# Optimization experiments

Measured on AMD Instinct MI355X. Metric: run time of the kernel, lower is better.

The kernel has to match this reference:

```python
import jax, jax.numpy as jnp
import numpy as np

N = 50000        # nodes
E = 1600000      # edges (before self-loops)
HID = 128
HEADS = 4
HD = HID // HEADS
FIN = 32 + 7     # node feats + scenario feats
EPS = 1e-5


def _ln(x, g, b):
    m = x.mean(-1, keepdims=True)
    v = ((x - m) ** 2).mean(-1, keepdims=True)
    return (x - m) / jnp.sqrt(v + EPS) * g + b


def _gat(x, src, dst, W, a_s, a_d, bias):
    # PyG GATConv (concat=True, negative_slope=0.2), eval mode (no dropout)
    xp = (x @ W).reshape(-1, HEADS, HD)                    # [N,H,C]
    es = (xp * a_s).sum(-1)                                # [N,H]
    ed = (xp * a_d).sum(-1)                                # [N,H]
    e = jax.nn.leaky_relu(es[src] + ed[dst], 0.2)          # [Etot,H]
    emax = jax.ops.segment_max(e, dst, num_segments=N)     # per-target softmax (self-loops guarantee nonempty segments)
    a = jnp.exp(e - emax[dst])
    denom = jax.ops.segment_sum(a, dst, num_segments=N)
    a = a / denom[dst]
    out = jax.ops.segment_sum(xp[src] * a[:, :, None], dst, num_segments=N)
    return out.reshape(-1, HID) + bias


def setup_inputs() -> dict:
    key = jax.random.key(0)
    ks = iter(jax.random.split(key, 64))

    def rn(shape, scale=0.05):
        return jax.random.normal(next(ks), shape, dtype=jnp.float32) * scale

    inp = {}
    inp["x"] = jax.random.normal(next(ks), (N, FIN), dtype=jnp.float32)
    inp["edge_index"] = jax.random.randint(next(ks), (2, E), 0, N)
    inp["enc_w1"] = rn((FIN, HID)); inp["enc_b1"] = jnp.zeros((HID,), jnp.float32)
    inp["enc_w2"] = rn((HID, HID)); inp["enc_b2"] = jnp.zeros((HID,), jnp.float32)
    for l in (1, 2, 3):
        inp[f"W{l}"] = rn((HID, HID))
        inp[f"as{l}"] = rn((HEADS, HD))
        inp[f"ad{l}"] = rn((HEADS, HD))
        inp[f"bc{l}"] = jnp.zeros((HID,), jnp.float32)
        inp[f"g{l}"] = jnp.ones((HID,), jnp.float32)
        inp[f"be{l}"] = jnp.zeros((HID,), jnp.float32)
    inp["imp_w1"] = rn((HID, HID // 2)); inp["imp_b1"] = jnp.zeros((HID // 2,), jnp.float32)
    inp["imp_w2"] = rn((HID // 2, 3));   inp["imp_b2"] = jnp.zeros((3,), jnp.float32)
    inp["tim_w1"] = rn((HID, HID // 2)); inp["tim_b1"] = jnp.zeros((HID // 2,), jnp.float32)
    inp["tim_w2"] = rn((HID // 2, 2));   inp["tim_b2"] = jnp.zeros((2,), jnp.float32)
    return inp


def reference(x, edge_index, enc_w1, enc_b1, enc_w2, enc_b2,
              W1, as1, ad1, bc1, g1, be1,
              W2, as2, ad2, bc2, g2, be2,
              W3, as3, ad3, bc3, g3, be3,
              imp_w1, imp_b1, imp_w2, imp_b2,
              tim_w1, tim_b1, tim_w2, tim_b2):
    loops = jnp.arange(N, dtype=edge_index.dtype)          # add_self_loops=True
    src = jnp.concatenate([edge_index[0], loops])
    dst = jnp.concatenate([edge_index[1], loops])
    h = jax.nn.relu(x @ enc_w1 + enc_b1) @ enc_w2 + enc_b2
    for (W, a_s, a_d, bc, g, be) in ((W1, as1, ad1, bc1, g1, be1),
                                     (W2, as2, ad2, bc2, g2, be2),
                                     (W3, as3, ad3, bc3, g3, be3)):
        h = jax.nn.relu(_ln(_gat(h, src, dst, W, a_s, a_d, bc) + h, g, be))
    impact = jax.nn.relu(h @ imp_w1 + imp_b1) @ imp_w2 + imp_b2
    timing = jax.nn.softplus(jax.nn.relu(h @ tim_w1 + tim_b1) @ tim_w2 + tim_b2)
    return (impact, timing)
```

## Files before the change

### kernel.cpp

```cpp
#include <hip/hip_runtime.h>
#include <hip/hip_bf16.h>
#include <math.h>

#define NN 50000
#define EDGES 1600000
#define ETOT (EDGES + NN)
#define FINDIM 39
#define NPART 256
#define PSZ 196
#define PCAP 7100
#define P1TILE 4096

typedef __attribute__((ext_vector_type(8))) short short8;
typedef __attribute__((ext_vector_type(4))) float floatx4;

__device__ __forceinline__ unsigned pack_bf16(float a, float b) {
    __hip_bfloat162 t;
    t.x = __float2bfloat16(a);
    t.y = __float2bfloat16(b);
    return *(unsigned*)&t;
}
__device__ __forceinline__ float2 unpack_bf16(unsigned w) {
    float2 r;
    r.x = __uint_as_float(w << 16);
    r.y = __uint_as_float(w & 0xffff0000u);
    return r;
}

__device__ __forceinline__ int src_at(const int* ei, int i, bool i32) {
    return i32 ? ei[i] : ei[2 * i];
}
__device__ __forceinline__ int dst_at(const int* ei, int i, bool i32) {
    return i32 ? ei[EDGES + i] : ei[2 * (EDGES + i)];
}

__global__ __launch_bounds__(1024) void pass1_kernel(const int* __restrict__ ei,
                                                     int* __restrict__ gcursor,
                                                     unsigned* __restrict__ pbuf) {
    __shared__ unsigned raw[P1TILE];
    __shared__ unsigned srt[P1TILE];
    __shared__ int pcnt[NPART], poff[NPART], pcur[NPART], gb[NPART];
    __shared__ int i32flag;
    int t = threadIdx.x;
    if (t == 0) i32flag = 0;
    __syncthreads();
    int chunk = (ETOT + gridDim.x - 1) / gridDim.x;
    int c0 = blockIdx.x * chunk;
    int c1 = c0 + chunk; if (c1 > ETOT) c1 = ETOT;
    int sb = c0 < EDGES - 64 ? c0 : 0;
    if (t < 64 && ei[2 * (sb + t) + 1] != 0) i32flag = 1;
    __syncthreads();
    bool i32 = (i32flag != 0);
    for (int t0 = c0; t0 < c1; t0 += P1TILE) {
        int tn = c1 - t0; if (tn > P1TILE) tn = P1TILE;
        if (t < NPART) { pcnt[t] = 0; pcur[t] = 0; }
        __syncthreads();
        for (int i = t; i < tn; i += 1024) {
            int e = t0 + i;
            int s, d;
            if (e < EDGES) { s = src_at(ei, e, i32); d = dst_at(ei, e, i32); }
            else { s = d = e - EDGES; }
            raw[i] = ((unsigned)s << 16) | (unsigned)d;
            atomicAdd(&pcnt[d / PSZ], 1);
        }
        __syncthreads();
        if (t < NPART) poff[t] = pcnt[t];
        __syncthreads();
        for (int off = 1; off < NPART; off <<= 1) {
            int v = (t < NPART && t >= off) ? poff[t - off] : 0;
            __syncthreads();
            if (t < NPART) poff[t] += v;
            __syncthreads();
        }
        if (t < NPART) {
            poff[t] -= pcnt[t];
            gb[t] = atomicAdd(&gcursor[t], pcnt[t]);
        }
        __syncthreads();
        for (int i = t; i < tn; i += 1024) {
            unsigned r = raw[i];
            int part = (int)(r & 0xFFFFu) / PSZ;
            int pos = poff[part] + atomicAdd(&pcur[part], 1);
            srt[pos] = r;
        }
        __syncthreads();
        for (int i = t; i < tn; i += 1024) {
            unsigned r = srt[i];
            int part = (int)(r & 0xFFFFu) / PSZ;
            int gpos = gb[part] + (i - poff[part]);
            if (gpos < PCAP) pbuf[(size_t)part * PCAP + gpos] = r;
        }
        __syncthreads();
    }
}

__global__ __launch_bounds__(1024) void pass2_kernel(const unsigned* __restrict__ pbuf,
                                                     const int* __restrict__ gcursor,
                                                     int* __restrict__ rowptr,
                                                     int* __restrict__ colidx) {
    __shared__ unsigned recs[PCAP];
    __shared__ int lhist[PSZ], lexcl[PSZ], lcur[PSZ];
    __shared__ int psm[NPART];
    int p = blockIdx.x;
    int t = threadIdx.x;
    if (t < NPART) psm[t] = gcursor[t];
    __syncthreads();
    for (int off = 1; off < NPART; off <<= 1) {
        int x = (t < NPART && t >= off) ? psm[t - off] : 0;
        __syncthreads();
        if (t < NPART) psm[t] += x;
        __syncthreads();
    }
    int n = gcursor[p]; if (n > PCAP) n = PCAP;
    int base = psm[p] - gcursor[p];
    if (p == NPART - 1 && t == 0) rowptr[NN] = psm[NPART - 1];
    int d0 = p * PSZ;
    int nd = NN - d0; if (nd > PSZ) nd = PSZ;
    if (nd < 0) nd = 0;
    for (int i = t; i < nd; i += 1024) { lhist[i] = 0; lcur[i] = 0; }
    __syncthreads();
    for (int i = t; i < n; i += 1024) {
        unsigned r = pbuf[(size_t)p * PCAP + i];
        recs[i] = r;
        atomicAdd(&lhist[(int)(r & 0xFFFFu) - d0], 1);
    }
    __syncthreads();
    for (int i = t; i < nd; i += 1024) lexcl[i] = lhist[i];
    __syncthreads();
    for (int off = 1; off < PSZ; off <<= 1) {
        int a0 = 0;
        if (t < nd && t >= off) a0 = lexcl[t - off];
        __syncthreads();
        if (t < nd) lexcl[t] += a0;
        __syncthreads();
    }
    for (int i = t; i < nd; i += 1024) {
        lexcl[i] -= lhist[i];
        rowptr[d0 + i] = base + lexcl[i];
    }
    __syncthreads();
    for (int i = t; i < n; i += 1024) {
        unsigned r = recs[i];
        int li = (int)(r & 0xFFFFu) - d0;
        int pos = base + lexcl[li] + atomicAdd(&lcur[li], 1);
        colidx[pos] = (int)(r >> 16);
    }
}

template <int NC, bool RELU, int K>
__global__ __launch_bounds__(256) void gemm_small_kernel(const float* __restrict__ A,
                                                         const float* __restrict__ B,
                                                         const float* __restrict__ bias,
                                                         float* __restrict__ C, int M) {
    constexpr int TM = 32;
    constexpr int GROUPS = 256 / NC;
    constexpr int RPG = TM / GROUPS;
    constexpr int KC = 64;
    __shared__ float As[TM * 128];
    __shared__ float Bs[KC * NC];
    int t = threadIdx.x;
    int i0 = blockIdx.x * TM;

    int rows = M - i0; if (rows > TM) rows = TM;
    for (int idx = t; idx < rows * K; idx += 256) {
        int r = idx / K, k = idx - r * K;
        As[r * K + k] = A[(size_t)(i0 + r) * K + k];
    }

    int col = t % NC, grp = t / NC;
    int rg0 = grp * RPG;
    float acc[RPG];
#pragma unroll
    for (int r = 0; r < RPG; ++r) acc[r] = 0.f;

    for (int k0 = 0; k0 < K; k0 += KC) {
        int kc = K - k0; if (kc > KC) kc = KC;
        __syncthreads();
        for (int idx = t; idx < kc * NC; idx += 256) Bs[idx] = B[(size_t)k0 * NC + idx];
        __syncthreads();
        for (int k = 0; k < kc; ++k) {
            float bv = Bs[k * NC + col];
#pragma unroll
            for (int r = 0; r < RPG; ++r) acc[r] += As[(rg0 + r) * K + k0 + k] * bv;
        }
    }

    float bb = bias ? bias[col] : 0.f;
#pragma unroll
    for (int r = 0; r < RPG; ++r) {
        int i = i0 + rg0 + r;
        if (i < M) {
            float v = acc[r] + bb;
            if (RELU) v = v > 0.f ? v : 0.f;
            C[(size_t)i * NC + col] = v;
        }
    }
}

__global__ __launch_bounds__(256) void wconv5_kernel(const float* __restrict__ W0,
                                                     const float* __restrict__ W1,
                                                     const float* __restrict__ W2,
                                                     const float* __restrict__ ew2,
                                                     const float* __restrict__ iw1,
                                                     const float* __restrict__ tw1,
                                                     unsigned short* __restrict__ wtb,
                                                     int* __restrict__ gcursor) {
    if (blockIdx.x == 0 && threadIdx.x < NPART) gcursor[threadIdx.x] = 0;
    int idx = blockIdx.x * 256 + threadIdx.x;
    int m = idx >> 14;
    int r = idx & 16383;
    int c = r >> 7, k = r & 127;
    float v;
    if (m == 0) v = W0[(size_t)k * 128 + c];
    else if (m == 1) v = W1[(size_t)k * 128 + c];
    else if (m == 2) v = W2[(size_t)k * 128 + c];
    else if (m == 3) v = ew2[(size_t)k * 128 + c];
    else v = (c < 64) ? iw1[(size_t)k * 64 + c] : tw1[(size_t)k * 64 + (c - 64)];
    unsigned p = pack_bf16(v, 0.f);
    wtb[idx] = (unsigned short)(p & 0xffffu);
}

__device__ __forceinline__ void mfma_core(const float* __restrict__ A, int arow, int valid,
                                          const unsigned short* __restrict__ wtb,
                                          int c, int grp, floatx4 acc[8]) {
#pragma unroll
    for (int n = 0; n < 8; ++n) acc[n] = (floatx4){0.f, 0.f, 0.f, 0.f};
    short8 af[4];
#pragma unroll
    for (int kc = 0; kc < 4; ++kc) {
        float4 f0 = make_float4(0.f, 0.f, 0.f, 0.f), f1 = f0;
        if (valid) {
            const float* hp = &A[(size_t)arow * 128 + (kc << 5) + (grp << 3)];
            f0 = *(const float4*)hp;
            f1 = *(const float4*)(hp + 4);
        }
        unsigned pk[4];
        pk[0] = pack_bf16(f0.x, f0.y);
        pk[1] = pack_bf16(f0.z, f0.w);
        pk[2] = pack_bf16(f1.x, f1.y);
        pk[3] = pack_bf16(f1.z, f1.w);
        af[kc] = *(short8*)pk;
    }
#pragma unroll
    for (int kc = 0; kc < 4; ++kc) {
#pragma unroll
        for (int n = 0; n < 8; ++n) {
            short8 bf = *(const short8*)&wtb[(size_t)(((n << 4) + c) * 128 + (kc << 5) + (grp << 3))];
            acc[n] = __builtin_amdgcn_mfma_f32_16x16x32_bf16(af[kc], bf, acc[n], 0, 0, 0);
        }
    }
}

__global__ __launch_bounds__(256) void gemm_mfma_kernel(const float* __restrict__ H,
                                                        const unsigned short* __restrict__ wtb,
                                                        unsigned* __restrict__ XP,
                                                        const float* __restrict__ a_s,
                                                        const float* __restrict__ a_d,
                                                        float* __restrict__ es,
                                                        float* __restrict__ ed, int M) {
    int t = threadIdx.x;
    int w = t >> 6, l = t & 63;
    int c = l & 15, grp = l >> 4;
    int i0 = blockIdx.x * 64 + w * 16;
    int arow = i0 + c;

    floatx4 acc[8];
    mfma_core(H, arow, arow < M, wtb, c, grp, acc);

    float asv[8], adv[8];
#pragma unroll
    for (int n = 0; n < 8; ++n) { asv[n] = a_s[(n << 4) + c]; adv[n] = a_d[(n << 4) + c]; }

    float sp[4][4], dp[4][4];
#pragma unroll
    for (int r = 0; r < 4; ++r)
#pragma unroll
        for (int hd = 0; hd < 4; ++hd) { sp[r][hd] = 0.f; dp[r][hd] = 0.f; }

#pragma unroll
    for (int n = 0; n < 8; ++n) {
#pragma unroll
        for (int r = 0; r < 4; ++r) {
            float vv = acc[n][r];
            float pv = __shfl_xor(vv, 1);
            int row = i0 + (grp << 2) + r;
            if (!(c & 1) && row < M)
                XP[(size_t)row * 64 + (n << 3) + (c >> 1)] = pack_bf16(vv, pv);
            sp[r][n >> 1] = fmaf(vv, asv[n], sp[r][n >> 1]);
            dp[r][n >> 1] = fmaf(vv, adv[n], dp[r][n >> 1]);
        }
    }
#pragma unroll
    for (int r = 0; r < 4; ++r)
#pragma unroll
        for (int hd = 0; hd < 4; ++hd) {
            float s = sp[r][hd], d = dp[r][hd];
#pragma unroll
            for (int off = 1; off <= 8; off <<= 1) {
                s += __shfl_xor(s, off);
                d += __shfl_xor(d, off);
            }
            sp[r][hd] = s; dp[r][hd] = d;
        }
    if (c < 4) {
#pragma unroll
        for (int r = 0; r < 4; ++r) {
            int row = i0 + (grp << 2) + r;
            if (row < M) {
                float s = (c == 0) ? sp[r][0] : (c == 1) ? sp[r][1] : (c == 2) ? sp[r][2] : sp[r][3];
                float d = (c == 0) ? dp[r][0] : (c == 1) ? dp[r][1] : (c == 2) ? dp[r][2] : dp[r][3];
                es[(size_t)row * 4 + c] = s;
                ed[(size_t)row * 4 + c] = d;
            }
        }
    }
}

__global__ __launch_bounds__(256) void gemm_mfma_bias_kernel(const float* __restrict__ A,
                                                             const unsigned short* __restrict__ wtb,
                                                             const float* __restrict__ bias,
                                                             float* __restrict__ C, int M) {
    int t = threadIdx.x;
    int w = t >> 6, l = t & 63;
    int c = l & 15, grp = l >> 4;
    int i0 = blockIdx.x * 64 + w * 16;
    int arow = i0 + c;

    floatx4 acc[8];
    mfma_core(A, arow, arow < M, wtb, c, grp, acc);

    float bv[8];
#pragma unroll
    for (int n = 0; n < 8; ++n) bv[n] = bias[(n << 4) + c];
#pragma unroll
    for (int n = 0; n < 8; ++n)
#pragma unroll
        for (int r = 0; r < 4; ++r) {
            int row = i0 + (grp << 2) + r;
            if (row < M) C[(size_t)row * 128 + (n << 4) + c] = acc[n][r] + bv[n];
        }
}

__global__ __launch_bounds__(256) void gemm_mfma_heads_kernel(const float* __restrict__ H,
                                                              const unsigned short* __restrict__ wtb,
                                                              const float* __restrict__ ib1,
                                                              const float* __restrict__ tb1,
                                                              const float* __restrict__ iw2,
                                                              const float* __restrict__ ib2,
                                                              const float* __restrict__ tw2,
                                                              const float* __restrict__ tb2,
                                                              float* __restrict__ out, int M) {
    int t = threadIdx.x;
    int w = t >> 6, l = t & 63;
    int c = l & 15, grp = l >> 4;
    int i0 = blockIdx.x * 64 + w * 16;
    int arow = i0 + c;

    floatx4 acc[8];
    mfma_core(H, arow, arow < M, wtb, c, grp, acc);

    float iw2v[4][3], tw2v[4][2], ib1v[4], tb1v[4];
#pragma unroll
    for (int n = 0; n < 4; ++n) {
        int lc = (n << 4) + c;
        ib1v[n] = ib1[lc];
        tb1v[n] = tb1[lc];
#pragma unroll
        for (int o = 0; o < 3; ++o) iw2v[n][o] = iw2[lc * 3 + o];
#pragma unroll
        for (int d = 0; d < 2; ++d) tw2v[n][d] = tw2[lc * 2 + d];
    }

    float pi[4][3], pt[4][2];
#pragma unroll
    for (int r = 0; r < 4; ++r) {
#pragma unroll
        for (int o = 0; o < 3; ++o) pi[r][o] = 0.f;
#pragma unroll
        for (int d = 0; d < 2; ++d) pt[r][d] = 0.f;
    }
#pragma unroll
    for (int n = 0; n < 4; ++n)
#pragma unroll
        for (int r = 0; r < 4; ++r) {
            float vi = acc[n][r] + ib1v[n];     vi = vi > 0.f ? vi : 0.f;
            float vt = acc[n + 4][r] + tb1v[n]; vt = vt > 0.f ? vt : 0.f;
#pragma unroll
            for (int o = 0; o < 3; ++o) pi[r][o] = fmaf(vi, iw2v[n][o], pi[r][o]);
#pragma unroll
            for (int d = 0; d < 2; ++d) pt[r][d] = fmaf(vt, tw2v[n][d], pt[r][d]);
        }
#pragma unroll
    for (int r = 0; r < 4; ++r) {
#pragma unroll
        for (int o = 0; o < 3; ++o) {
            float s = pi[r][o];
#pragma unroll
            for (int off = 1; off <= 8; off <<= 1) s += __shfl_xor(s, off);
            pi[r][o] = s;
        }
#pragma unroll
        for (int d = 0; d < 2; ++d) {
            float s = pt[r][d];
#pragma unroll
            for (int off = 1; off <= 8; off <<= 1) s += __shfl_xor(s, off);
            pt[r][d] = s;
        }
    }
    if (c == 0) {
#pragma unroll
        for (int r = 0; r < 4; ++r) {
            int row = i0 + (grp << 2) + r;
            if (row < M) {
#pragma unroll
                for (int o = 0; o < 3; ++o) out[(size_t)row * 3 + o] = pi[r][o] + ib2[o];
#pragma unroll
                for (int d = 0; d < 2; ++d) {
                    float a = pt[r][d] + tb2[d];
                    float sp = a > 20.f ? a : log1pf(__expf(a));
                    out[(size_t)(NN * 3) + (size_t)row * 2 + d] = sp;
                }
            }
        }
    }
}

__global__ __launch_bounds__(256, 6) void gat_kernel(const unsigned* __restrict__ xpk,
                                                     const float* __restrict__ es,
                                                     const float* __restrict__ ed,
                                                     const int* __restrict__ rowptr,
                                                     const int* __restrict__ colidx,
                                                     float* __restrict__ h,
                                                     const float* __restrict__ bc,
                                                     const float* __restrict__ g,
                                                     const float* __restrict__ be) {
    int wv = threadIdx.x >> 6, l = threadIdx.x & 63;
    int hf = l >> 5;
    int lh = l & 31;
    int hd = lh >> 3;
    int j  = lh & 7;
    int v = blockIdx.x * 8 + wv * 2 + hf;
    if (v >= NN) return;
    int s0 = rowptr[v], s1 = rowptr[v + 1];
    int len = s1 - s0;
    int nmax = max(len, __shfl_xor(len, 32));
    int c0 = (hd << 5) + (j << 2);
    int xsel = (hd << 4) + (j << 1);
    float edv = ed[((unsigned)v << 2) + hd];

    float4 h4 = *(const float4*)&h[(size_t)v * 128 + c0];

    float a0 = 0.f, a1 = 0.f, a2 = 0.f, a3 = 0.f, den = 0.f;
    for (int p8 = 0; p8 < nmax; p8 += 8) {
        int u[8];
#pragma unroll
        for (int q = 0; q < 8; ++q) {
            int idx = p8 + q;
            u[q] = colidx[s0 + (idx < len ? idx : len - 1)];
        }
        uint2 xw[8];
#pragma unroll
        for (int q = 0; q < 8; ++q)
            xw[q] = *(const uint2*)&xpk[((unsigned)u[q] << 6) + xsel];
        float w[8];
#pragma unroll
        for (int q = 0; q < 8; ++q) {
            float e = es[((unsigned)u[q] << 2) + hd] + edv;
            e = fmaxf(e, 0.2f * e);
            float ww = __expf(e);
            w[q] = (p8 + q < len) ? ww : 0.f;
            den += w[q];
        }
#pragma unroll
        for (int q = 0; q < 8; ++q) {
            float2 x0 = unpack_bf16(xw[q].x);
            float2 x1 = unpack_bf16(xw[q].y);
            a0 = fmaf(w[q], x0.x, a0);
            a1 = fmaf(w[q], x0.y, a1);
            a2 = fmaf(w[q], x1.x, a2);
            a3 = fmaf(w[q], x1.y, a3);
        }
    }
    float rd = 1.f / den;

    float4 bc4 = *(const float4*)&bc[c0];
    float y0 = a0 * rd + bc4.x + h4.x;
    float y1 = a1 * rd + bc4.y + h4.y;
    float y2 = a2 * rd + bc4.z + h4.z;
    float y3 = a3 * rd + bc4.w + h4.w;

    float s = y0 + y1 + y2 + y3;
#pragma unroll
    for (int off = 16; off >= 1; off >>= 1) s += __shfl_xor(s, off);
    float mean = s * (1.f / 128.f);
    float d0 = y0 - mean, d1 = y1 - mean, d2 = y2 - mean, d3 = y3 - mean;
    float vv = d0 * d0 + d1 * d1 + d2 * d2 + d3 * d3;
#pragma unroll
    for (int off = 16; off >= 1; off >>= 1) vv += __shfl_xor(vv, off);
    float rstd = rsqrtf(vv * (1.f / 128.f) + 1e-5f);
    float4 g4  = *(const float4*)&g[c0];
    float4 be4 = *(const float4*)&be[c0];
    float z0 = d0 * rstd * g4.x + be4.x;
    float z1 = d1 * rstd * g4.y + be4.y;
    float z2 = d2 * rstd * g4.z + be4.z;
    float z3 = d3 * rstd * g4.w + be4.w;
    float4 o;
    o.x = z0 > 0.f ? z0 : 0.f;
    o.y = z1 > 0.f ? z1 : 0.f;
    o.z = z2 > 0.f ? z2 : 0.f;
    o.w = z3 > 0.f ? z3 : 0.f;
    *(float4*)&h[(size_t)v * 128 + c0] = o;
}

extern "C" void kernel_launch(void* const* d_in, const int* in_sizes, int n_in,
                              void* d_out, int out_size, void* d_ws, size_t ws_size,
                              hipStream_t stream) {
    const float* x      = (const float*)d_in[0];
    const int*   ei     = (const int*)d_in[1];
    const float* enc_w1 = (const float*)d_in[2];
    const float* enc_b1 = (const float*)d_in[3];
    const float* enc_w2 = (const float*)d_in[4];
    const float* enc_b2 = (const float*)d_in[5];
    const float *W[3], *as_[3], *ad_[3], *bc[3], *g[3], *be[3];
    for (int l = 0; l < 3; ++l) {
        W[l]   = (const float*)d_in[6 + l * 6 + 0];
        as_[l] = (const float*)d_in[6 + l * 6 + 1];
        ad_[l] = (const float*)d_in[6 + l * 6 + 2];
        bc[l]  = (const float*)d_in[6 + l * 6 + 3];
        g[l]   = (const float*)d_in[6 + l * 6 + 4];
        be[l]  = (const float*)d_in[6 + l * 6 + 5];
    }
    const float* imp_w1 = (const float*)d_in[24];
    const float* imp_b1 = (const float*)d_in[25];
    const float* imp_w2 = (const float*)d_in[26];
    const float* imp_b2 = (const float*)d_in[27];
    const float* tim_w1 = (const float*)d_in[28];
    const float* tim_b1 = (const float*)d_in[29];
    const float* tim_w2 = (const float*)d_in[30];
    const float* tim_b2 = (const float*)d_in[31];

    int* gcursor = (int*)d_ws;
    int* rowptr  = gcursor + NPART + 64;
    int* colidx  = rowptr + NN + 1;
    uintptr_t pb = (uintptr_t)(colidx + ETOT + 8);
    pb = (pb + 255) & ~(uintptr_t)255;
    unsigned* pbuf = (unsigned*)pb;
    uintptr_t fb = (uintptr_t)(pbuf + (size_t)NPART * PCAP);
    fb = (fb + 255) & ~(uintptr_t)255;
    float* es = (float*)fb;
    float* ed = es + (size_t)NN * 4;
    float* h  = ed + (size_t)NN * 4;
    float* xpf = h + (size_t)NN * 128;
    unsigned* xpk = (unsigned*)xpf;
    unsigned short* wtb = (unsigned short*)(xpf + (size_t)NN * 128);
    float* tmp = xpf;

    wconv5_kernel<<<320, 256, 0, stream>>>(W[0], W[1], W[2], enc_w2, imp_w1, tim_w1, wtb, gcursor);
    pass1_kernel<<<512, 1024, 0, stream>>>(ei, gcursor, pbuf);
    pass2_kernel<<<NPART, 1024, 0, stream>>>(pbuf, gcursor, rowptr, colidx);

    const int GB64 = (NN + 63) / 64;
    gemm_small_kernel<128, true, FINDIM><<<(NN + 31) / 32, 256, 0, stream>>>(x, enc_w1, enc_b1, tmp, NN);
    gemm_mfma_bias_kernel<<<GB64, 256, 0, stream>>>(tmp, wtb + (size_t)3 * 16384, enc_b2, h, NN);

    for (int l = 0; l < 3; ++l) {
        gemm_mfma_kernel<<<GB64, 256, 0, stream>>>(h, wtb + (size_t)l * 16384, xpk,
                                                   as_[l], ad_[l], es, ed, NN);
        gat_kernel<<<(NN + 7) / 8, 256, 0, stream>>>(xpk, es, ed, rowptr, colidx, h,
                                                     bc[l], g[l], be[l]);
    }

    gemm_mfma_heads_kernel<<<GB64, 256, 0, stream>>>(h, wtb + (size_t)4 * 16384,
                                                     imp_b1, tim_b1, imp_w2, imp_b2,
                                                     tim_w2, tim_b2, (float*)d_out, NN);
}
```

Measured before the change: 510.8 us.

## Pad CSR rows to multiples of eight with sentinel node, fold weight conversion into pass2

Replaces rowptr with a packed per-row descriptor (slab offset plus padded length) and pads each adjacency row to a multiple of 8 using a sentinel node whose features are zero and score is -1e30. The GAT loop then drops per-edge bounds checks and masking. It also removes the global prefix scan in pass2 by using fixed per-partition slabs, moves the weight bf16 conversion into pass2, and replaces the cursor-clearing kernel with a memset. The costs are extra padded gathers, a row-length cap of 2040, and a layout that relies on offsets fitting in 24 bits.

Measured after the change: 507.7 us. About the same (-0.6%).

```diff
diff --git a/kernel.cpp b/kernel.cpp
--- a/kernel.cpp
+++ b/kernel.cpp
@@ -9,6 +9,7 @@
 #define NPART 256
 #define PSZ 196
 #define PCAP 7100
+#define PCAP_PAD 8480
 #define P1TILE 4096
 
 typedef __attribute__((ext_vector_type(8))) short short8;
@@ -96,24 +97,21 @@
 
 __global__ __launch_bounds__(1024) void pass2_kernel(const unsigned* __restrict__ pbuf,
                                                      const int* __restrict__ gcursor,
-                                                     int* __restrict__ rowptr,
-                                                     int* __restrict__ colidx) {
+                                                     unsigned* __restrict__ rowdesc,
+                                                     int* __restrict__ colidx,
+                                                     const float* __restrict__ W0,
+                                                     const float* __restrict__ W1,
+                                                     const float* __restrict__ W2,
+                                                     const float* __restrict__ ew2,
+                                                     const float* __restrict__ iw1,
+                                                     const float* __restrict__ tw1,
+                                                     unsigned short* __restrict__ wtb) {
     __shared__ unsigned recs[PCAP];
     __shared__ int lhist[PSZ], lexcl[PSZ], lcur[PSZ];
-    __shared__ int psm[NPART];
     int p = blockIdx.x;
     int t = threadIdx.x;
-    if (t < NPART) psm[t] = gcursor[t];
-    __syncthreads();
-    for (int off = 1; off < NPART; off <<= 1) {
-        int x = (t < NPART && t >= off) ? psm[t - off] : 0;
-        __syncthreads();
-        if (t < NPART) psm[t] += x;
-        __syncthreads();
-    }
     int n = gcursor[p]; if (n > PCAP) n = PCAP;
-    int base = psm[p] - gcursor[p];
-    if (p == NPART - 1 && t == 0) rowptr[NN] = psm[NPART - 1];
+    int slab = p * PCAP_PAD;
     int d0 = p * PSZ;
     int nd = NN - d0; if (nd > PSZ) nd = PSZ;
     if (nd < 0) nd = 0;
@@ -125,7 +123,7 @@
         atomicAdd(&lhist[(int)(r & 0xFFFFu) - d0], 1);
     }
     __syncthreads();
-    for (int i = t; i < nd; i += 1024) lexcl[i] = lhist[i];
+    for (int i = t; i < nd; i += 1024) lexcl[i] = min((lhist[i] + 7) & ~7, 2040);
     __syncthreads();
     for (int off = 1; off < PSZ; off <<= 1) {
         int a0 = 0;
@@ -135,15 +133,35 @@
         __syncthreads();
     }
     for (int i = t; i < nd; i += 1024) {
-        lexcl[i] -= lhist[i];
-        rowptr[d0 + i] = base + lexcl[i];
+        int pl = min((lhist[i] + 7) & ~7, 2040);
+        lexcl[i] -= pl;
+        rowdesc[d0 + i] = (unsigned)(slab + lexcl[i]) | ((unsigned)(pl >> 3) << 24);
     }
     __syncthreads();
     for (int i = t; i < n; i += 1024) {
         unsigned r = recs[i];
         int li = (int)(r & 0xFFFFu) - d0;
-        int pos = base + lexcl[li] + atomicAdd(&lcur[li], 1);
+        int pos = slab + lexcl[li] + atomicAdd(&lcur[li], 1);
         colidx[pos] = (int)(r >> 16);
+    }
+    for (int i = t; i < nd; i += 1024) {
+        int pl = min((lhist[i] + 7) & ~7, 2040);
+        int base = slab + lexcl[i];
+        for (int k = lhist[i]; k < pl; ++k) colidx[base + k] = NN;
+    }
+    int widx = p * 1024 + t;
+    if (widx < 5 * 16384) {
+        int m = widx >> 14;
+        int r = widx & 16383;
+        int c = r >> 7, k = r & 127;
+        float v;
+        if (m == 0) v = W0[(size_t)k * 128 + c];
+        else if (m == 1) v = W1[(size_t)k * 128 + c];
+        else if (m == 2) v = W2[(size_t)k * 128 + c];
+        else if (m == 3) v = ew2[(size_t)k * 128 + c];
+        else v = (c < 64) ? iw1[(size_t)k * 64 + c] : tw1[(size_t)k * 64 + (c - 64)];
+        unsigned pk = pack_bf16(v, 0.f);
+        wtb[widx] = (unsigned short)(pk & 0xffffu);
     }
 }
 
@@ -197,29 +215,6 @@
     }
 }
 
-__global__ __launch_bounds__(256) void wconv5_kernel(const float* __restrict__ W0,
-                                                     const float* __restrict__ W1,
-                                                     const float* __restrict__ W2,
-                                                     const float* __restrict__ ew2,
-                                                     const float* __restrict__ iw1,
-                                                     const float* __restrict__ tw1,
-                                                     unsigned short* __restrict__ wtb,
-                                                     int* __restrict__ gcursor) {
-    if (blockIdx.x == 0 && threadIdx.x < NPART) gcursor[threadIdx.x] = 0;
-    int idx = blockIdx.x * 256 + threadIdx.x;
-    int m = idx >> 14;
-    int r = idx & 16383;
-    int c = r >> 7, k = r & 127;
-    float v;
-    if (m == 0) v = W0[(size_t)k * 128 + c];
-    else if (m == 1) v = W1[(size_t)k * 128 + c];
-    else if (m == 2) v = W2[(size_t)k * 128 + c];
-    else if (m == 3) v = ew2[(size_t)k * 128 + c];
-    else v = (c < 64) ? iw1[(size_t)k * 64 + c] : tw1[(size_t)k * 64 + (c - 64)];
-    unsigned p = pack_bf16(v, 0.f);
-    wtb[idx] = (unsigned short)(p & 0xffffu);
-}
-
 __device__ __forceinline__ void mfma_core(const float* __restrict__ A, int arow, int valid,
                                           const unsigned short* __restrict__ wtb,
                                           int c, int grp, floatx4 acc[8]) {
@@ -263,6 +258,11 @@
     int c = l & 15, grp = l >> 4;
     int i0 = blockIdx.x * 64 + w * 16;
     int arow = i0 + c;
+
+    if (blockIdx.x == 0) {
+        if (t < 64) XP[(size_t)NN * 64 + t] = 0u;
+        else if (t < 68) es[(size_t)NN * 4 + (t - 64)] = -1e30f;
+    }
 
     floatx4 acc[8];
     mfma_core(H, arow, arow < M, wtb, c, grp, acc);
@@ -428,7 +428,7 @@
 __global__ __launch_bounds__(256, 6) void gat_kernel(const unsigned* __restrict__ xpk,
                                                      const float* __restrict__ es,
                                                      const float* __restrict__ ed,
-                                                     const int* __restrict__ rowptr,
+                                                     const unsigned* __restrict__ rowdesc,
                                                      const int* __restrict__ colidx,
                                                      float* __restrict__ h,
                                                      const float* __restrict__ bc,
@@ -441,9 +441,9 @@
     int j  = lh & 7;
     int v = blockIdx.x * 8 + wv * 2 + hf;
     if (v >= NN) return;
-    int s0 = rowptr[v], s1 = rowptr[v + 1];
-    int len = s1 - s0;
-    int nmax = max(len, __shfl_xor(len, 32));
+    unsigned dsc = rowdesc[v];
+    int s0 = (int)(dsc & 0xFFFFFFu);
+    int alen = (int)(dsc >> 24) << 3;
     int c0 = (hd << 5) + (j << 2);
     int xsel = (hd << 4) + (j << 1);
     float edv = ed[((unsigned)v << 2) + hd];
@@ -451,13 +451,10 @@
     float4 h4 = *(const float4*)&h[(size_t)v * 128 + c0];
 
     float a0 = 0.f, a1 = 0.f, a2 = 0.f, a3 = 0.f, den = 0.f;
-    for (int p8 = 0; p8 < nmax; p8 += 8) {
+    for (int p8 = 0; p8 < alen; p8 += 8) {
         int u[8];
 #pragma unroll
-        for (int q = 0; q < 8; ++q) {
-            int idx = p8 + q;
-            u[q] = colidx[s0 + (idx < len ? idx : len - 1)];
-        }
+        for (int q = 0; q < 8; ++q) u[q] = colidx[s0 + p8 + q];
         uint2 xw[8];
 #pragma unroll
         for (int q = 0; q < 8; ++q)
@@ -467,8 +464,7 @@
         for (int q = 0; q < 8; ++q) {
             float e = es[((unsigned)u[q] << 2) + hd] + edv;
             e = fmaxf(e, 0.2f * e);
-            float ww = __expf(e);
-            w[q] = (p8 + q < len) ? ww : 0.f;
+            w[q] = __expf(e);
             den += w[q];
         }
 #pragma unroll
@@ -540,24 +536,25 @@
     const float* tim_b2 = (const float*)d_in[31];
 
     int* gcursor = (int*)d_ws;
-    int* rowptr  = gcursor + NPART + 64;
-    int* colidx  = rowptr + NN + 1;
-    uintptr_t pb = (uintptr_t)(colidx + ETOT + 8);
+    unsigned* rowdesc = (unsigned*)(gcursor + NPART + 64);
+    int* colidx = (int*)(rowdesc + NN);
+    uintptr_t pb = (uintptr_t)(colidx + (size_t)NPART * PCAP_PAD);
     pb = (pb + 255) & ~(uintptr_t)255;
     unsigned* pbuf = (unsigned*)pb;
     uintptr_t fb = (uintptr_t)(pbuf + (size_t)NPART * PCAP);
     fb = (fb + 255) & ~(uintptr_t)255;
     float* es = (float*)fb;
-    float* ed = es + (size_t)NN * 4;
+    float* ed = es + (size_t)NN * 4 + 64;
     float* h  = ed + (size_t)NN * 4;
     float* xpf = h + (size_t)NN * 128;
     unsigned* xpk = (unsigned*)xpf;
     unsigned short* wtb = (unsigned short*)(xpf + (size_t)NN * 128);
     float* tmp = xpf;
 
-    wconv5_kernel<<<320, 256, 0, stream>>>(W[0], W[1], W[2], enc_w2, imp_w1, tim_w1, wtb, gcursor);
+    hipMemsetAsync(gcursor, 0, NPART * sizeof(int), stream);
     pass1_kernel<<<512, 1024, 0, stream>>>(ei, gcursor, pbuf);
-    pass2_kernel<<<NPART, 1024, 0, stream>>>(pbuf, gcursor, rowptr, colidx);
+    pass2_kernel<<<NPART, 1024, 0, stream>>>(pbuf, gcursor, rowdesc, colidx,
+                                             W[0], W[1], W[2], enc_w2, imp_w1, tim_w1, wtb);
 
     const int GB64 = (NN + 63) / 64;
     gemm_small_kernel<128, true, FINDIM><<<(NN + 31) / 32, 256, 0, stream>>>(x, enc_w1, enc_b1, tmp, NN);
@@ -566,7 +563,7 @@
     for (int l = 0; l < 3; ++l) {
         gemm_mfma_kernel<<<GB64, 256, 0, stream>>>(h, wtb + (size_t)l * 16384, xpk,
                                                    as_[l], ad_[l], es, ed, NN);
-        gat_kernel<<<(NN + 7) / 8, 256, 0, stream>>>(xpk, es, ed, rowptr, colidx, h,
+        gat_kernel<<<(NN + 7) / 8, 256, 0, stream>>>(xpk, es, ed, rowdesc, colidx, h,
                                                      bc[l], g[l], be[l]);
     }
 
```
